# Kernel optimization log

Hardware: AMD Instinct MI355X
Metric: run time of the kernel (lower is better)

The kernel has to match this reference:

```python
import jax, jax.numpy as jnp
import numpy as np

B, S, D, H = 2, 2048, 1024, 16
HD = D // H  # head_dim = 64


def setup_inputs() -> dict:
    key = jax.random.key(0)
    ks = jax.random.split(key, 12)
    scale = 1.0 / np.sqrt(D)
    inp = {
        "query": jax.random.normal(ks[0], (B, S, D), jnp.float32),
        "key": jax.random.normal(ks[1], (B, S, D), jnp.float32),
        "value": jax.random.normal(ks[2], (B, S, D), jnp.float32),
        # causal mask, broadcast over batch and heads; masked_fill where mask == 0
        "mask": jnp.tril(jnp.ones((1, 1, S, S), dtype=bool)),
        "Wq": jax.random.normal(ks[3], (D, D), jnp.float32) * scale,
        "bq": jax.random.normal(ks[4], (D,), jnp.float32) * scale,
        "Wk": jax.random.normal(ks[5], (D, D), jnp.float32) * scale,
        "bk": jax.random.normal(ks[6], (D,), jnp.float32) * scale,
        "Wv": jax.random.normal(ks[7], (D, D), jnp.float32) * scale,
        "bv": jax.random.normal(ks[8], (D,), jnp.float32) * scale,
        "Wo": jax.random.normal(ks[9], (D, D), jnp.float32) * scale,
        "bo": jax.random.normal(ks[10], (D,), jnp.float32) * scale,
    }
    return inp


def reference(query, key, value, mask, Wq, bq, Wk, bk, Wv, bv, Wo, bo):
    b = query.shape[0]
    # QKV projections -> [B, H, S, HD]
    q = (query @ Wq + bq).reshape(b, -1, H, HD).transpose(0, 2, 1, 3)
    k = (key @ Wk + bk).reshape(b, -1, H, HD).transpose(0, 2, 1, 3)
    v = (value @ Wv + bv).reshape(b, -1, H, HD).transpose(0, 2, 1, 3)
    # scores: [B, H, Sq, Sk]
    scores = jnp.einsum("bhqd,bhkd->bhqk", q, k) / jnp.sqrt(jnp.float32(HD))
    scores = jnp.where(mask, scores, jnp.float32(-1e9))
    attn = jax.nn.softmax(scores, axis=-1)
    # dropout is identity in eval mode
    ctx = jnp.einsum("bhqk,bhkd->bhqd", attn, v)  # [B, H, Sq, HD]
    concat = ctx.transpose(0, 2, 1, 3).reshape(b, -1, D)
    return concat @ Wo + bo
```

## Files before the change

### kernel.cpp

```cpp
#include <hip/hip_runtime.h>

#define B_ 2
#define S_ 2048
#define D_ 1024
#define H_ 16
#define HD_ 64
#define Msz (B_*S_)

typedef __attribute__((ext_vector_type(8))) short  short8v;
typedef __attribute__((ext_vector_type(4))) float  float4v;
typedef __attribute__((ext_vector_type(4))) unsigned int uint4v;

__device__ static __forceinline__ unsigned short f2bf(float x) {
    union { float f; unsigned u; } v; v.f = x;
    unsigned r = v.u + 0x7fffu + ((v.u >> 16) & 1u);
    return (unsigned short)(r >> 16);
}
__device__ static __forceinline__ float bf2f(unsigned short b) {
    union { float f; unsigned u; } v; v.u = ((unsigned)b) << 16;
    return v.f;
}
__device__ static __forceinline__ void split2(float x, unsigned short& hi, unsigned short& lo) {
    hi = f2bf(x);
    lo = f2bf(x - bf2f(hi));
}

__device__ static __forceinline__ void gl_lds16(const void* g, void* l) {
    __builtin_amdgcn_global_load_lds(
        (const __attribute__((address_space(1))) void*)g,
        (__attribute__((address_space(3))) void*)l, 16, 0, 0);
}

__global__ __launch_bounds__(256) void conv_split(
    const float* __restrict__ in, unsigned short* __restrict__ hi,
    unsigned short* __restrict__ lo, int n4)
{
    const int i = blockIdx.x * 256 + threadIdx.x;
    if (i >= n4) return;
    const float4 x = ((const float4*)in)[i];
    ushort4 h, l;
    split2(x.x, h.x, l.x);
    split2(x.y, h.y, l.y);
    split2(x.z, h.z, l.z);
    split2(x.w, h.w, l.w);
    ((ushort4*)hi)[i] = h;
    ((ushort4*)lo)[i] = l;
}

__global__ __launch_bounds__(256) void conv_split_T(
    const float* __restrict__ W, unsigned short* __restrict__ thi,
    unsigned short* __restrict__ tlo, int R, int C)
{
    __shared__ float t[32][33];
    const int tid = threadIdx.x;
    const int r8 = tid >> 5, c = tid & 31;
    const int kbase = blockIdx.y * 32;
    const int nbase = blockIdx.x * 32;
#pragma unroll
    for (int i = 0; i < 4; ++i)
        t[r8 + i*8][c] = W[(size_t)(kbase + r8 + i*8) * C + nbase + c];
    __syncthreads();
#pragma unroll
    for (int i = 0; i < 4; ++i) {
        const int rr = r8 + i*8;
        const float v = t[c][rr];
        unsigned short h, l; split2(v, h, l);
        thi[(size_t)(nbase + rr) * R + kbase + c] = h;
        tlo[(size_t)(nbase + rr) * R + kbase + c] = l;
    }
}

__global__ __launch_bounds__(256) void gemm_mfma_split(
    const unsigned short* __restrict__ Ahi, const unsigned short* __restrict__ Alo,
    const unsigned short* __restrict__ Bthi, const unsigned short* __restrict__ Btlo,
    const float* __restrict__ bias, float* __restrict__ out,
    unsigned short* __restrict__ ohi, unsigned short* __restrict__ olo,
    int M, int N, int K, int mode, float scale)
{
    __shared__ unsigned short Ah[128][40], Al[128][40], Bh[64][40], Bl[64][40];

    const int tid  = threadIdx.x;
    const int lane = tid & 63;
    const int wave = tid >> 6;
    const int wr = wave >> 1, wc = wave & 1;
    const int m0 = blockIdx.x * 128, n0 = blockIdx.y * 64;

    float4v acc[4][2];
#pragma unroll
    for (int mi = 0; mi < 4; ++mi)
#pragma unroll
        for (int ni = 0; ni < 2; ++ni)
#pragma unroll
            for (int r = 0; r < 4; ++r) acc[mi][ni][r] = 0.f;

    const int mrow = lane & 15;
    const int kb8  = (lane >> 4) * 8;

    for (int k0 = 0; k0 < K; k0 += 32) {
        __syncthreads();
#pragma unroll
        for (int c2 = 0; c2 < 2; ++c2) {
            const int id  = tid + c2*256;
            const int row = id >> 2, ko = (id & 3) * 8;
            *(short8v*)&Ah[row][ko] = *(const short8v*)&Ahi[(size_t)(m0+row)*K + k0 + ko];
            *(short8v*)&Al[row][ko] = *(const short8v*)&Alo[(size_t)(m0+row)*K + k0 + ko];
        }
        {
            const int row = tid >> 2, ko = (tid & 3) * 8;
            *(short8v*)&Bh[row][ko] = *(const short8v*)&Bthi[(size_t)(n0+row)*K + k0 + ko];
            *(short8v*)&Bl[row][ko] = *(const short8v*)&Btlo[(size_t)(n0+row)*K + k0 + ko];
        }
        __syncthreads();

        short8v af[4][2], bfr[2][2];
#pragma unroll
        for (int mi = 0; mi < 4; ++mi) {
            af[mi][0] = *(const short8v*)&Ah[wr*64 + mi*16 + mrow][kb8];
            af[mi][1] = *(const short8v*)&Al[wr*64 + mi*16 + mrow][kb8];
        }
#pragma unroll
        for (int ni = 0; ni < 2; ++ni) {
            bfr[ni][0] = *(const short8v*)&Bh[wc*32 + ni*16 + mrow][kb8];
            bfr[ni][1] = *(const short8v*)&Bl[wc*32 + ni*16 + mrow][kb8];
        }
#pragma unroll
        for (int mi = 0; mi < 4; ++mi)
#pragma unroll
            for (int ni = 0; ni < 2; ++ni) {
                acc[mi][ni] = __builtin_amdgcn_mfma_f32_16x16x32_bf16(af[mi][0], bfr[ni][0], acc[mi][ni], 0, 0, 0);
                acc[mi][ni] = __builtin_amdgcn_mfma_f32_16x16x32_bf16(af[mi][0], bfr[ni][1], acc[mi][ni], 0, 0, 0);
                acc[mi][ni] = __builtin_amdgcn_mfma_f32_16x16x32_bf16(af[mi][1], bfr[ni][0], acc[mi][ni], 0, 0, 0);
            }
    }

    const int rbase = (lane >> 4) * 4, cidx = lane & 15;
#pragma unroll
    for (int mi = 0; mi < 4; ++mi)
#pragma unroll
        for (int ni = 0; ni < 2; ++ni) {
            const int col = n0 + wc*32 + ni*16 + cidx;
            const float bv = bias[col];
#pragma unroll
            for (int r = 0; r < 4; ++r) {
                const int row = m0 + wr*64 + mi*16 + rbase + r;
                const float v = (acc[mi][ni][r] + bv) * scale;
                if (mode == 0) {
                    out[(size_t)row * N + col] = v;
                } else {
                    const int bb = row >> 11;
                    const int ss = row & (S_ - 1);
                    const int hh = col >> 6;
                    const int hd = col & (HD_ - 1);
                    const size_t o = (((size_t)(bb*H_ + hh) * S_) + ss) * HD_ + hd;
                    unsigned short hb, lb; split2(v, hb, lb);
                    ohi[o] = hb;
                    olo[o] = lb;
                }
            }
        }
}

__global__ __launch_bounds__(256) void transpose_v(
    const unsigned short* __restrict__ V, unsigned short* __restrict__ Vt)
{
    __shared__ unsigned tbuf[64][33];
    const int tid = threadIdx.x;
    const int head = blockIdx.y;
    const int s0 = blockIdx.x * 64;
    const unsigned short* src = V + (size_t)head * S_ * HD_;
    unsigned short* dst = Vt + (size_t)head * HD_ * S_;

    const int sp = tid >> 3;
    const int dch = tid & 7;
    const short8v a = *(const short8v*)&src[(size_t)(s0 + 2*sp    ) * HD_ + dch*8];
    const short8v b = *(const short8v*)&src[(size_t)(s0 + 2*sp + 1) * HD_ + dch*8];
#pragma unroll
    for (int j = 0; j < 8; ++j) {
        const unsigned lo = (unsigned short)a[j];
        const unsigned hi = (unsigned short)b[j];
        tbuf[dch*8 + j][sp] = lo | (hi << 16);
    }
    __syncthreads();
#pragma unroll
    for (int i = 0; i < 2; ++i) {
        const int c = i*256 + tid;
        const int d = c >> 3, ch = c & 7;
        uint4v o;
#pragma unroll
        for (int k = 0; k < 4; ++k) o[k] = tbuf[d][ch*4 + k];
        *(uint4v*)&dst[(size_t)d * S_ + s0 + ch*8] = o;
    }
}

__global__ __launch_bounds__(256) void attn_mfma(
    const unsigned short* __restrict__ Qhi, const unsigned short* __restrict__ Qlo,
    const unsigned short* __restrict__ Khi, const unsigned short* __restrict__ Klo,
    const unsigned short* __restrict__ Vt,
    unsigned short* __restrict__ Chi, unsigned short* __restrict__ Clo)
{
    __shared__ unsigned short Ks[2][2][64][64];
    __shared__ unsigned short Vs[2][64][64];
    __shared__ unsigned short Ps[4][32][64];

    const int tid = threadIdx.x, lane = tid & 63, w = tid >> 6;
    const int bid = blockIdx.x;
    const int head = bid & 31;
    const int qb = ((bid >> 5) + head) & 15;
    const int q0 = qb * 128;

    const size_t hQK = (size_t)head * S_ * HD_;
    const unsigned short* Qh = Qhi + hQK;
    const unsigned short* Ql = Qlo + hQK;
    const unsigned short* Kh = Khi + hQK;
    const unsigned short* Kl = Klo + hQK;
    const unsigned short* Vth = Vt + (size_t)head * HD_ * S_;

    const int fr = lane & 15;
    const int fk = (lane >> 4) * 8;
    const int xorE = (lane & 7) * 8;
    const int rbase = (lane >> 4) * 4;

    short8v qf[2][2][2];
#pragma unroll
    for (int mi = 0; mi < 2; ++mi)
#pragma unroll
        for (int ks = 0; ks < 2; ++ks) {
            const size_t off = (size_t)(q0 + w*32 + mi*16 + fr) * HD_ + ks*32 + fk;
            qf[mi][ks][0] = *(const short8v*)&Qh[off];
            qf[mi][ks][1] = *(const short8v*)&Ql[off];
        }

    float4v oacc[2][4];
#pragma unroll
    for (int mi = 0; mi < 2; ++mi)
#pragma unroll
        for (int dt = 0; dt < 4; ++dt)
#pragma unroll
            for (int r = 0; r < 4; ++r) oacc[mi][dt][r] = 0.f;
    float m_run[2][4], l_run[2][4];
#pragma unroll
    for (int mi = 0; mi < 2; ++mi)
#pragma unroll
        for (int r = 0; r < 4; ++r) { m_run[mi][r] = -3.0e38f; l_run[mi][r] = 0.f; }

    const int srow = lane >> 3;
    const int sxor = ((lane & 7) ^ srow) * 8;

    const int ntiles = 2*qb + 2;
    const int last_t = 2*qb + (w >> 1);

    auto stage = [&](int t, int buf) {
#pragma unroll
        for (int cc = 0; cc < 6; ++cc) {
            const int c = w*6 + cc;
            if (c < 8) {
                gl_lds16(&Kh[(size_t)(t*64 + c*8 + srow)*HD_ + sxor], &Ks[buf][0][c*8][0]);
            } else if (c < 16) {
                const int c2 = c - 8;
                gl_lds16(&Kl[(size_t)(t*64 + c2*8 + srow)*HD_ + sxor], &Ks[buf][1][c2*8][0]);
            } else {
                const int c2 = c - 16;
                gl_lds16(&Vth[(size_t)(c2*8 + srow)*S_ + t*64 + sxor], &Vs[buf][c2*8][0]);
            }
        }
    };

    stage(0, 0);
    int buf = 0;
    for (int t = 0; t < ntiles; ++t) {
        if (t + 1 < ntiles) {
            stage(t + 1, buf ^ 1);
            asm volatile("s_waitcnt vmcnt(6)" ::: "memory");
        } else {
            asm volatile("s_waitcnt vmcnt(0)" ::: "memory");
        }
        __builtin_amdgcn_s_barrier();
        __builtin_amdgcn_sched_barrier(0);

        if (t <= last_t) {
            float4v sacc[2][4];
#pragma unroll
            for (int mi = 0; mi < 2; ++mi)
#pragma unroll
                for (int ni = 0; ni < 4; ++ni)
#pragma unroll
                    for (int r = 0; r < 4; ++r) sacc[mi][ni][r] = 0.f;
#pragma unroll
            for (int ks = 0; ks < 2; ++ks)
#pragma unroll
                for (int ni = 0; ni < 4; ++ni) {
                    const short8v kh = *(const short8v*)&Ks[buf][0][ni*16 + fr][(ks*32 + fk) ^ xorE];
                    const short8v kl = *(const short8v*)&Ks[buf][1][ni*16 + fr][(ks*32 + fk) ^ xorE];
#pragma unroll
                    for (int mi = 0; mi < 2; ++mi) {
                        sacc[mi][ni] = __builtin_amdgcn_mfma_f32_16x16x32_bf16(qf[mi][ks][0], kh, sacc[mi][ni], 0, 0, 0);
                        sacc[mi][ni] = __builtin_amdgcn_mfma_f32_16x16x32_bf16(qf[mi][ks][1], kh, sacc[mi][ni], 0, 0, 0);
                        sacc[mi][ni] = __builtin_amdgcn_mfma_f32_16x16x32_bf16(qf[mi][ks][0], kl, sacc[mi][ni], 0, 0, 0);
                    }
                }

            const int kvb = t*64;
            if (kvb + 63 > q0 + w*32) {
#pragma unroll
                for (int mi = 0; mi < 2; ++mi)
#pragma unroll
                    for (int ni = 0; ni < 4; ++ni)
#pragma unroll
                        for (int r = 0; r < 4; ++r) {
                            const int row_g = q0 + w*32 + mi*16 + rbase + r;
                            const int col_g = kvb + ni*16 + fr;
                            if (col_g > row_g) sacc[mi][ni][r] = -1.0e9f;
                        }
            }

            float tmax[2][4];
#pragma unroll
            for (int mi = 0; mi < 2; ++mi)
#pragma unroll
                for (int r = 0; r < 4; ++r)
                    tmax[mi][r] = fmaxf(fmaxf(sacc[mi][0][r], sacc[mi][1][r]),
                                        fmaxf(sacc[mi][2][r], sacc[mi][3][r]));
#pragma unroll
            for (int d = 1; d <= 8; d <<= 1)
#pragma unroll
                for (int mi = 0; mi < 2; ++mi)
#pragma unroll
                    for (int r = 0; r < 4; ++r)
                        tmax[mi][r] = fmaxf(tmax[mi][r], __shfl_xor(tmax[mi][r], d, 64));
#pragma unroll
            for (int mi = 0; mi < 2; ++mi)
#pragma unroll
                for (int r = 0; r < 4; ++r) {
                    const float mnew = fmaxf(m_run[mi][r], tmax[mi][r]);
                    const float sc = __expf(m_run[mi][r] - mnew);
                    m_run[mi][r] = mnew;
                    l_run[mi][r] *= sc;
#pragma unroll
                    for (int dt = 0; dt < 4; ++dt) oacc[mi][dt][r] *= sc;
                }
#pragma unroll
            for (int mi = 0; mi < 2; ++mi)
#pragma unroll
                for (int ni = 0; ni < 4; ++ni)
#pragma unroll
                    for (int r = 0; r < 4; ++r) {
                        const float p = __expf(sacc[mi][ni][r] - m_run[mi][r]);
                        const unsigned short pb = f2bf(p);
                        l_run[mi][r] += bf2f(pb);
                        const int R = mi*16 + rbase + r;
                        Ps[w][R][(ni*16 + fr) ^ ((R & 7) * 8)] = pb;
                    }

#pragma unroll
            for (int ks = 0; ks < 2; ++ks) {
                short8v pa[2];
#pragma unroll
                for (int mi = 0; mi < 2; ++mi)
                    pa[mi] = *(const short8v*)&Ps[w][mi*16 + fr][(ks*32 + fk) ^ xorE];
#pragma unroll
                for (int dt = 0; dt < 4; ++dt) {
                    const short8v vf = *(const short8v*)&Vs[buf][dt*16 + fr][(ks*32 + fk) ^ xorE];
#pragma unroll
                    for (int mi = 0; mi < 2; ++mi)
                        oacc[mi][dt] = __builtin_amdgcn_mfma_f32_16x16x32_bf16(pa[mi], vf, oacc[mi][dt], 0, 0, 0);
                }
            }
        }

        __builtin_amdgcn_s_barrier();
        buf ^= 1;
    }

#pragma unroll
    for (int d = 1; d <= 8; d <<= 1)
#pragma unroll
        for (int mi = 0; mi < 2; ++mi)
#pragma unroll
            for (int r = 0; r < 4; ++r)
                l_run[mi][r] += __shfl_xor(l_run[mi][r], d, 64);

    const int b = head >> 4, h = head & 15;
#pragma unroll
    for (int mi = 0; mi < 2; ++mi)
#pragma unroll
        for (int r = 0; r < 4; ++r) {
            const float inv = 1.0f / l_run[mi][r];
            const int sg = q0 + w*32 + mi*16 + rbase + r;
            const size_t rb = ((size_t)(b * S_ + sg)) * D_ + h * 64;
#pragma unroll
            for (int dt = 0; dt < 4; ++dt) {
                const float v = oacc[mi][dt][r] * inv;
                unsigned short hb, lb; split2(v, hb, lb);
                Chi[rb + dt*16 + fr] = hb;
                Clo[rb + dt*16 + fr] = lb;
            }
        }
}

extern "C" void kernel_launch(void* const* d_in, const int* in_sizes, int n_in,
                              void* d_out, int out_size, void* d_ws, size_t ws_size,
                              hipStream_t stream)
{
    const float* query = (const float*)d_in[0];
    const float* key   = (const float*)d_in[1];
    const float* value = (const float*)d_in[2];
    const float* Wq = (const float*)d_in[4];
    const float* bq = (const float*)d_in[5];
    const float* Wk = (const float*)d_in[6];
    const float* bk = (const float*)d_in[7];
    const float* Wv = (const float*)d_in[8];
    const float* bv = (const float*)d_in[9];
    const float* Wo = (const float*)d_in[10];
    const float* bo = (const float*)d_in[11];
    float* out = (float*)d_out;

    const size_t nElem = (size_t)B_ * S_ * D_;
    char* wsb = (char*)d_ws;
    unsigned short* Xhi = (unsigned short*)(wsb + 0);
    unsigned short* Xlo = (unsigned short*)(wsb + 8ull*1024*1024);
    unsigned short* Qph = (unsigned short*)(wsb + 16ull*1024*1024);
    unsigned short* Qpl = (unsigned short*)(wsb + 24ull*1024*1024);
    unsigned short* Kph = (unsigned short*)(wsb + 32ull*1024*1024);
    unsigned short* Kpl = (unsigned short*)(wsb + 40ull*1024*1024);
    unsigned short* Vph = (unsigned short*)(wsb + 48ull*1024*1024);
    unsigned short* Vpl = (unsigned short*)(wsb + 56ull*1024*1024);
    unsigned short* Wph = (unsigned short*)(wsb + 64ull*1024*1024);
    unsigned short* Wpl = (unsigned short*)(wsb + 66ull*1024*1024);
    unsigned short* VtT = Xhi;
    unsigned short* Chi = Vph;
    unsigned short* Clo = Vpl;

    const dim3 cblk(256);
    const dim3 cgrd(nElem / 1024);
    const dim3 tgrd(D_/32, D_/32);
    const dim3 ggrd(Msz/128, D_/64);
    const dim3 vtgrd(S_/64, B_*H_);
    const dim3 agrd(B_ * H_ * (S_/128));

    const float iscale = 0.125f;

    conv_split<<<cgrd, cblk, 0, stream>>>(query, Xhi, Xlo, (int)(nElem/4));
    conv_split_T<<<tgrd, cblk, 0, stream>>>(Wq, Wph, Wpl, D_, D_);
    gemm_mfma_split<<<ggrd, cblk, 0, stream>>>(Xhi, Xlo, Wph, Wpl, bq, nullptr, Qph, Qpl, Msz, D_, D_, 1, iscale);
    conv_split<<<cgrd, cblk, 0, stream>>>(key, Xhi, Xlo, (int)(nElem/4));
    conv_split_T<<<tgrd, cblk, 0, stream>>>(Wk, Wph, Wpl, D_, D_);
    gemm_mfma_split<<<ggrd, cblk, 0, stream>>>(Xhi, Xlo, Wph, Wpl, bk, nullptr, Kph, Kpl, Msz, D_, D_, 1, 1.0f);
    conv_split<<<cgrd, cblk, 0, stream>>>(value, Xhi, Xlo, (int)(nElem/4));
    conv_split_T<<<tgrd, cblk, 0, stream>>>(Wv, Wph, Wpl, D_, D_);
    gemm_mfma_split<<<ggrd, cblk, 0, stream>>>(Xhi, Xlo, Wph, Wpl, bv, nullptr, Vph, Vpl, Msz, D_, D_, 1, 1.0f);
    transpose_v<<<vtgrd, cblk, 0, stream>>>(Vph, VtT);
    attn_mfma<<<agrd, cblk, 0, stream>>>(Qph, Qpl, Kph, Kpl, VtT, Chi, Clo);
    conv_split_T<<<tgrd, cblk, 0, stream>>>(Wo, Wph, Wpl, D_, D_);
    gemm_mfma_split<<<ggrd, cblk, 0, stream>>>(Chi, Clo, Wph, Wpl, bo, out, nullptr, nullptr, Msz, D_, D_, 0, 1.0f);
}
```

Before: 421.8 us.

## Fuse fp32-to-bf16 split into GEMM A loads and widen GEMM tile to 128x128

Removes the separate conv_split kernels for query, key and value. The QKV GEMMs now read fp32 activations directly and split them into truncated-hi plus rounded-lo bf16 pairs while filling LDS. The GEMM tile also grows from 128x64 to 128x128, with each wave covering a 64x64 sub-tile, to raise reuse per LDS load. Together this drops three kernel launches and the intermediate hi/lo write and read-back. In exchange it uses more registers and LDS per block and launches half as many blocks, and the truncated hi split changes rounding slightly.

```diff
diff --git a/kernel.cpp b/kernel.cpp
--- a/kernel.cpp
+++ b/kernel.cpp
@@ -24,27 +24,16 @@
     hi = f2bf(x);
     lo = f2bf(x - bf2f(hi));
 }
+__device__ static __forceinline__ void split2t(float x, unsigned short& hi, unsigned short& lo) {
+    union { float f; unsigned u; } v; v.f = x;
+    hi = (unsigned short)(v.u >> 16);
+    lo = f2bf(x - bf2f(hi));
+}
 
 __device__ static __forceinline__ void gl_lds16(const void* g, void* l) {
     __builtin_amdgcn_global_load_lds(
         (const __attribute__((address_space(1))) void*)g,
         (__attribute__((address_space(3))) void*)l, 16, 0, 0);
-}
-
-__global__ __launch_bounds__(256) void conv_split(
-    const float* __restrict__ in, unsigned short* __restrict__ hi,
-    unsigned short* __restrict__ lo, int n4)
-{
-    const int i = blockIdx.x * 256 + threadIdx.x;
-    if (i >= n4) return;
-    const float4 x = ((const float4*)in)[i];
-    ushort4 h, l;
-    split2(x.x, h.x, l.x);
-    split2(x.y, h.y, l.y);
-    split2(x.z, h.z, l.z);
-    split2(x.w, h.w, l.w);
-    ((ushort4*)hi)[i] = h;
-    ((ushort4*)lo)[i] = l;
 }
 
 __global__ __launch_bounds__(256) void conv_split_T(
@@ -70,66 +59,90 @@
     }
 }
 
-__global__ __launch_bounds__(256) void gemm_mfma_split(
-    const unsigned short* __restrict__ Ahi, const unsigned short* __restrict__ Alo,
+template<int AMODE>
+__global__ __launch_bounds__(256) void gemm_mfma2(
+    const float* __restrict__ Af,
+    const unsigned short* __restrict__ Aphi, const unsigned short* __restrict__ Aplo,
     const unsigned short* __restrict__ Bthi, const unsigned short* __restrict__ Btlo,
     const float* __restrict__ bias, float* __restrict__ out,
     unsigned short* __restrict__ ohi, unsigned short* __restrict__ olo,
     int M, int N, int K, int mode, float scale)
 {
-    __shared__ unsigned short Ah[128][40], Al[128][40], Bh[64][40], Bl[64][40];
+    __shared__ __align__(16) unsigned short Ah[128][40], Al[128][40];
+    __shared__ __align__(16) unsigned short Bh[128][40], Bl[128][40];
 
     const int tid  = threadIdx.x;
     const int lane = tid & 63;
     const int wave = tid >> 6;
     const int wr = wave >> 1, wc = wave & 1;
-    const int m0 = blockIdx.x * 128, n0 = blockIdx.y * 64;
-
-    float4v acc[4][2];
+    const int m0 = blockIdx.x * 128, n0 = blockIdx.y * 128;
+
+    float4v acc[4][4];
 #pragma unroll
     for (int mi = 0; mi < 4; ++mi)
 #pragma unroll
-        for (int ni = 0; ni < 2; ++ni)
+        for (int ni = 0; ni < 4; ++ni)
 #pragma unroll
             for (int r = 0; r < 4; ++r) acc[mi][ni][r] = 0.f;
 
-    const int mrow = lane & 15;
-    const int kb8  = (lane >> 4) * 8;
+    const int fr  = lane & 15;
+    const int kb8 = (lane >> 4) * 8;
 
     for (int k0 = 0; k0 < K; k0 += 32) {
         __syncthreads();
-#pragma unroll
-        for (int c2 = 0; c2 < 2; ++c2) {
-            const int id  = tid + c2*256;
-            const int row = id >> 2, ko = (id & 3) * 8;
-            *(short8v*)&Ah[row][ko] = *(const short8v*)&Ahi[(size_t)(m0+row)*K + k0 + ko];
-            *(short8v*)&Al[row][ko] = *(const short8v*)&Alo[(size_t)(m0+row)*K + k0 + ko];
-        }
-        {
-            const int row = tid >> 2, ko = (tid & 3) * 8;
-            *(short8v*)&Bh[row][ko] = *(const short8v*)&Bthi[(size_t)(n0+row)*K + k0 + ko];
-            *(short8v*)&Bl[row][ko] = *(const short8v*)&Btlo[(size_t)(n0+row)*K + k0 + ko];
+        if (AMODE == 0) {
+#pragma unroll
+            for (int it = 0; it < 4; ++it) {
+                const int id  = tid + it*256;
+                const int row = id >> 3;
+                const int kq  = (id & 7) * 4;
+                const float4 f = *(const float4*)&Af[(size_t)(m0+row)*K + k0 + kq];
+                ushort4 h, l;
+                split2t(f.x, h.x, l.x);
+                split2t(f.y, h.y, l.y);
+                split2t(f.z, h.z, l.z);
+                split2t(f.w, h.w, l.w);
+                *(ushort4*)&Ah[row][kq] = h;
+                *(ushort4*)&Al[row][kq] = l;
+            }
+        } else {
+#pragma unroll
+            for (int it = 0; it < 2; ++it) {
+                const int id  = tid + it*256;
+                const int row = id >> 2;
+                const int kc  = (id & 3) * 8;
+                *(short8v*)&Ah[row][kc] = *(const short8v*)&Aphi[(size_t)(m0+row)*K + k0 + kc];
+                *(short8v*)&Al[row][kc] = *(const short8v*)&Aplo[(size_t)(m0+row)*K + k0 + kc];
+            }
+        }
+#pragma unroll
+        for (int it = 0; it < 2; ++it) {
+            const int id  = tid + it*256;
+            const int row = id >> 2;
+            const int kc  = (id & 3) * 8;
+            *(short8v*)&Bh[row][kc] = *(const short8v*)&Bthi[(size_t)(n0+row)*K + k0 + kc];
+            *(short8v*)&Bl[row][kc] = *(const short8v*)&Btlo[(size_t)(n0+row)*K + k0 + kc];
         }
         __syncthreads();
 
-        short8v af[4][2], bfr[2][2];
+        short8v af[4][2], bf[4][2];
 #pragma unroll
         for (int mi = 0; mi < 4; ++mi) {
-            af[mi][0] = *(const short8v*)&Ah[wr*64 + mi*16 + mrow][kb8];
-            af[mi][1] = *(const short8v*)&Al[wr*64 + mi*16 + mrow][kb8];
-        }
-#pragma unroll
-        for (int ni = 0; ni < 2; ++ni) {
-            bfr[ni][0] = *(const short8v*)&Bh[wc*32 + ni*16 + mrow][kb8];
-            bfr[ni][1] = *(const short8v*)&Bl[wc*32 + ni*16 + mrow][kb8];
+            af[mi][0] = *(const short8v*)&Ah[wr*64 + mi*16 + fr][kb8];
+            af[mi][1] = *(const short8v*)&Al[wr*64 + mi*16 + fr][kb8];
+        }
+#pragma unroll
+        for (int ni = 0; ni < 4; ++ni) {
+            bf[ni][0] = *(const short8v*)&Bh[wc*64 + ni*16 + fr][kb8];
+            bf[ni][1] = *(const short8v*)&Bl[wc*64 + ni*16 + fr][kb8];
         }
 #pragma unroll
         for (int mi = 0; mi < 4; ++mi)
 #pragma unroll
-            for (int ni = 0; ni < 2; ++ni) {
-                acc[mi][ni] = __builtin_amdgcn_mfma_f32_16x16x32_bf16(af[mi][0], bfr[ni][0], acc[mi][ni], 0, 0, 0);
-                acc[mi][ni] = __builtin_amdgcn_mfma_f32_16x16x32_bf16(af[mi][0], bfr[ni][1], acc[mi][ni], 0, 0, 0);
-                acc[mi][ni] = __builtin_amdgcn_mfma_f32_16x16x32_bf16(af[mi][1], bfr[ni][0], acc[mi][ni], 0, 0, 0);
+            for (int ni = 0; ni < 4; ++ni) {
+                acc[mi][ni] = __builtin_amdgcn_mfma_f32_16x16x32_bf16(af[mi][0], bf[ni][0], acc[mi][ni], 0, 0, 0);
+                acc[mi][ni] = __builtin_amdgcn_mfma_f32_16x16x32_bf16(af[mi][0], bf[ni][1], acc[mi][ni], 0, 0, 0);
+                acc[mi][ni] = __builtin_amdgcn_mfma_f32_16x16x32_bf16(af[mi][1], bf[ni][0], acc[mi][ni], 0, 0, 0);
             }
     }
 
@@ -137,8 +150,8 @@
 #pragma unroll
     for (int mi = 0; mi < 4; ++mi)
 #pragma unroll
-        for (int ni = 0; ni < 2; ++ni) {
-            const int col = n0 + wc*32 + ni*16 + cidx;
+        for (int ni = 0; ni < 4; ++ni) {
+            const int col = n0 + wc*64 + ni*16 + cidx;
             const float bv = bias[col];
 #pragma unroll
             for (int r = 0; r < 4; ++r) {
@@ -414,42 +427,39 @@
     const float* bo = (const float*)d_in[11];
     float* out = (float*)d_out;
 
-    const size_t nElem = (size_t)B_ * S_ * D_;
     char* wsb = (char*)d_ws;
-    unsigned short* Xhi = (unsigned short*)(wsb + 0);
-    unsigned short* Xlo = (unsigned short*)(wsb + 8ull*1024*1024);
-    unsigned short* Qph = (unsigned short*)(wsb + 16ull*1024*1024);
-    unsigned short* Qpl = (unsigned short*)(wsb + 24ull*1024*1024);
-    unsigned short* Kph = (unsigned short*)(wsb + 32ull*1024*1024);
-    unsigned short* Kpl = (unsigned short*)(wsb + 40ull*1024*1024);
-    unsigned short* Vph = (unsigned short*)(wsb + 48ull*1024*1024);
-    unsigned short* Vpl = (unsigned short*)(wsb + 56ull*1024*1024);
-    unsigned short* Wph = (unsigned short*)(wsb + 64ull*1024*1024);
-    unsigned short* Wpl = (unsigned short*)(wsb + 66ull*1024*1024);
-    unsigned short* VtT = Xhi;
+    unsigned short* Qph = (unsigned short*)(wsb + 0);
+    unsigned short* Qpl = (unsigned short*)(wsb + 8ull*1024*1024);
+    unsigned short* Kph = (unsigned short*)(wsb + 16ull*1024*1024);
+    unsigned short* Kpl = (unsigned short*)(wsb + 24ull*1024*1024);
+    unsigned short* Vph = (unsigned short*)(wsb + 32ull*1024*1024);
+    unsigned short* Vpl = (unsigned short*)(wsb + 40ull*1024*1024);
+    unsigned short* VtT = (unsigned short*)(wsb + 48ull*1024*1024);
+    unsigned short* Wph = (unsigned short*)(wsb + 56ull*1024*1024);
+    unsigned short* Wpl = (unsigned short*)(wsb + 58ull*1024*1024);
     unsigned short* Chi = Vph;
     unsigned short* Clo = Vpl;
 
     const dim3 cblk(256);
-    const dim3 cgrd(nElem / 1024);
     const dim3 tgrd(D_/32, D_/32);
-    const dim3 ggrd(Msz/128, D_/64);
+    const dim3 ggrd(Msz/128, D_/128);
     const dim3 vtgrd(S_/64, B_*H_);
     const dim3 agrd(B_ * H_ * (S_/128));
 
     const float iscale = 0.125f;
 
-    conv_split<<<cgrd, cblk, 0, stream>>>(query, Xhi, Xlo, (int)(nElem/4));
     conv_split_T<<<tgrd, cblk, 0, stream>>>(Wq, Wph, Wpl, D_, D_);
-    gemm_mfma_split<<<ggrd, cblk, 0, stream>>>(Xhi, Xlo, Wph, Wpl, bq, nullptr, Qph, Qpl, Msz, D_, D_, 1, iscale);
-    conv_split<<<cgrd, cblk, 0, stream>>>(key, Xhi, Xlo, (int)(nElem/4));
+    gemm_mfma2<0><<<ggrd, cblk, 0, stream>>>(query, nullptr, nullptr, Wph, Wpl, bq,
+                                             nullptr, Qph, Qpl, Msz, D_, D_, 1, iscale);
     conv_split_T<<<tgrd, cblk, 0, stream>>>(Wk, Wph, Wpl, D_, D_);
-    gemm_mfma_split<<<ggrd, cblk, 0, stream>>>(Xhi, Xlo, Wph, Wpl, bk, nullptr, Kph, Kpl, Msz, D_, D_, 1, 1.0f);
-    conv_split<<<cgrd, cblk, 0, stream>>>(value, Xhi, Xlo, (int)(nElem/4));
+    gemm_mfma2<0><<<ggrd, cblk, 0, stream>>>(key, nullptr, nullptr, Wph, Wpl, bk,
+                                             nullptr, Kph, Kpl, Msz, D_, D_, 1, 1.0f);
     conv_split_T<<<tgrd, cblk, 0, stream>>>(Wv, Wph, Wpl, D_, D_);
-    gemm_mfma_split<<<ggrd, cblk, 0, stream>>>(Xhi, Xlo, Wph, Wpl, bv, nullptr, Vph, Vpl, Msz, D_, D_, 1, 1.0f);
+    gemm_mfma2<0><<<ggrd, cblk, 0, stream>>>(value, nullptr, nullptr, Wph, Wpl, bv,
+                                             nullptr, Vph, Vpl, Msz, D_, D_, 1, 1.0f);
     transpose_v<<<vtgrd, cblk, 0, stream>>>(Vph, VtT);
     attn_mfma<<<agrd, cblk, 0, stream>>>(Qph, Qpl, Kph, Kpl, VtT, Chi, Clo);
     conv_split_T<<<tgrd, cblk, 0, stream>>>(Wo, Wph, Wpl, D_, D_);
-    gemm_mfma_split<<<ggrd, cblk, 0, stream>>>(Chi, Clo, Wph, Wpl, bo, out, nullptr, nullptr, Msz, D_, D_, 0, 1.0f);
-}
+    gemm_mfma2<1><<<ggrd, cblk, 0, stream>>>(nullptr, Chi, Clo, Wph, Wpl, bo,
+                                             out, nullptr, nullptr, Msz, D_, D_, 0, 1.0f);
+}
```

New measurement: 477.4 us. 1.13x slower.

## Rewrite split-bf16 GEMM with 128x128 tiles, direct global-to-LDS loads and XOR swizzle

Applied to the files above, without the earlier changes.

Replaces the projection GEMM with a 512-thread kernel that uses 128x128 output tiles and a K step of 64. Operands go from global memory straight into LDS through a gl_lds16 helper, and an XOR-swizzled layout is meant to avoid bank conflicts. The aim is fewer blocks, more reuse of each loaded tile, and fewer load instructions and barriers per K. The helper gl_lds16 is not defined in the shown diff, so the change depends on it already existing; there is still no double buffering.

```diff
diff --git a/kernel.cpp b/kernel.cpp
--- a/kernel.cpp
+++ b/kernel.cpp
@@ -70,20 +70,21 @@
     }
 }
 
-__global__ __launch_bounds__(256) void gemm_mfma_split(
-    const unsigned short* __restrict__ Ahi, const unsigned short* __restrict__ Alo,
+__global__ __launch_bounds__(512) void gemm3(
+    const unsigned short* __restrict__ Aphi, const unsigned short* __restrict__ Aplo,
     const unsigned short* __restrict__ Bthi, const unsigned short* __restrict__ Btlo,
     const float* __restrict__ bias, float* __restrict__ out,
     unsigned short* __restrict__ ohi, unsigned short* __restrict__ olo,
     int M, int N, int K, int mode, float scale)
 {
-    __shared__ unsigned short Ah[128][40], Al[128][40], Bh[64][40], Bl[64][40];
+    __shared__ __align__(16) unsigned short Ah[128][64], Al[128][64];
+    __shared__ __align__(16) unsigned short Bh[128][64], Bl[128][64];
 
     const int tid  = threadIdx.x;
     const int lane = tid & 63;
-    const int wave = tid >> 6;
-    const int wr = wave >> 1, wc = wave & 1;
-    const int m0 = blockIdx.x * 128, n0 = blockIdx.y * 64;
+    const int w    = tid >> 6;
+    const int wr = w >> 2, wc = w & 3;
+    const int m0 = blockIdx.x * 128, n0 = blockIdx.y * 128;
 
     float4v acc[4][2];
 #pragma unroll
@@ -93,44 +94,56 @@
 #pragma unroll
             for (int r = 0; r < 4; ++r) acc[mi][ni][r] = 0.f;
 
-    const int mrow = lane & 15;
-    const int kb8  = (lane >> 4) * 8;
-
-    for (int k0 = 0; k0 < K; k0 += 32) {
+    const int fr   = lane & 15;
+    const int fk   = (lane >> 4) * 8;
+    const int xorE = (lane & 7) * 8;
+    const int srow = lane >> 3;
+    const int sxor = ((lane & 7) ^ srow) * 8;
+
+    const int bufsel = w >> 1;
+    const int gbase  = (w & 1) * 8;
+
+    for (int k0 = 0; k0 < K; k0 += 64) {
+#pragma unroll
+        for (int i = 0; i < 8; ++i) {
+            const int row0 = (gbase + i) * 8;
+            const int grow = row0 + srow;
+            if (bufsel == 0)
+                gl_lds16(&Aphi[(size_t)(m0+grow)*K + k0 + sxor], &Ah[row0][0]);
+            else if (bufsel == 1)
+                gl_lds16(&Aplo[(size_t)(m0+grow)*K + k0 + sxor], &Al[row0][0]);
+            else if (bufsel == 2)
+                gl_lds16(&Bthi[(size_t)(n0+grow)*K + k0 + sxor], &Bh[row0][0]);
+            else
+                gl_lds16(&Btlo[(size_t)(n0+grow)*K + k0 + sxor], &Bl[row0][0]);
+        }
         __syncthreads();
-#pragma unroll
-        for (int c2 = 0; c2 < 2; ++c2) {
-            const int id  = tid + c2*256;
-            const int row = id >> 2, ko = (id & 3) * 8;
-            *(short8v*)&Ah[row][ko] = *(const short8v*)&Ahi[(size_t)(m0+row)*K + k0 + ko];
-            *(short8v*)&Al[row][ko] = *(const short8v*)&Alo[(size_t)(m0+row)*K + k0 + ko];
-        }
-        {
-            const int row = tid >> 2, ko = (tid & 3) * 8;
-            *(short8v*)&Bh[row][ko] = *(const short8v*)&Bthi[(size_t)(n0+row)*K + k0 + ko];
-            *(short8v*)&Bl[row][ko] = *(const short8v*)&Btlo[(size_t)(n0+row)*K + k0 + ko];
+
+#pragma unroll
+        for (int ks = 0; ks < 2; ++ks) {
+            short8v af[4][2], bf[2][2];
+#pragma unroll
+            for (int mi = 0; mi < 4; ++mi) {
+                const int row = wr*64 + mi*16 + fr;
+                af[mi][0] = *(const short8v*)&Ah[row][(ks*32 + fk) ^ xorE];
+                af[mi][1] = *(const short8v*)&Al[row][(ks*32 + fk) ^ xorE];
+            }
+#pragma unroll
+            for (int ni = 0; ni < 2; ++ni) {
+                const int row = wc*32 + ni*16 + fr;
+                bf[ni][0] = *(const short8v*)&Bh[row][(ks*32 + fk) ^ xorE];
+                bf[ni][1] = *(const short8v*)&Bl[row][(ks*32 + fk) ^ xorE];
+            }
+#pragma unroll
+            for (int mi = 0; mi < 4; ++mi)
+#pragma unroll
+                for (int ni = 0; ni < 2; ++ni) {
+                    acc[mi][ni] = __builtin_amdgcn_mfma_f32_16x16x32_bf16(af[mi][0], bf[ni][0], acc[mi][ni], 0, 0, 0);
+                    acc[mi][ni] = __builtin_amdgcn_mfma_f32_16x16x32_bf16(af[mi][0], bf[ni][1], acc[mi][ni], 0, 0, 0);
+                    acc[mi][ni] = __builtin_amdgcn_mfma_f32_16x16x32_bf16(af[mi][1], bf[ni][0], acc[mi][ni], 0, 0, 0);
+                }
         }
         __syncthreads();
-
-        short8v af[4][2], bfr[2][2];
-#pragma unroll
-        for (int mi = 0; mi < 4; ++mi) {
-            af[mi][0] = *(const short8v*)&Ah[wr*64 + mi*16 + mrow][kb8];
-            af[mi][1] = *(const short8v*)&Al[wr*64 + mi*16 + mrow][kb8];
-        }
-#pragma unroll
-        for (int ni = 0; ni < 2; ++ni) {
-            bfr[ni][0] = *(const short8v*)&Bh[wc*32 + ni*16 + mrow][kb8];
-            bfr[ni][1] = *(const short8v*)&Bl[wc*32 + ni*16 + mrow][kb8];
-        }
-#pragma unroll
-        for (int mi = 0; mi < 4; ++mi)
-#pragma unroll
-            for (int ni = 0; ni < 2; ++ni) {
-                acc[mi][ni] = __builtin_amdgcn_mfma_f32_16x16x32_bf16(af[mi][0], bfr[ni][0], acc[mi][ni], 0, 0, 0);
-                acc[mi][ni] = __builtin_amdgcn_mfma_f32_16x16x32_bf16(af[mi][0], bfr[ni][1], acc[mi][ni], 0, 0, 0);
-                acc[mi][ni] = __builtin_amdgcn_mfma_f32_16x16x32_bf16(af[mi][1], bfr[ni][0], acc[mi][ni], 0, 0, 0);
-            }
     }
 
     const int rbase = (lane >> 4) * 4, cidx = lane & 15;
@@ -431,9 +444,10 @@
     unsigned short* Clo = Vpl;
 
     const dim3 cblk(256);
+    const dim3 gblk(512);
     const dim3 cgrd(nElem / 1024);
     const dim3 tgrd(D_/32, D_/32);
-    const dim3 ggrd(Msz/128, D_/64);
+    const dim3 ggrd(Msz/128, D_/128);
     const dim3 vtgrd(S_/64, B_*H_);
     const dim3 agrd(B_ * H_ * (S_/128));
 
@@ -441,15 +455,15 @@
 
     conv_split<<<cgrd, cblk, 0, stream>>>(query, Xhi, Xlo, (int)(nElem/4));
     conv_split_T<<<tgrd, cblk, 0, stream>>>(Wq, Wph, Wpl, D_, D_);
-    gemm_mfma_split<<<ggrd, cblk, 0, stream>>>(Xhi, Xlo, Wph, Wpl, bq, nullptr, Qph, Qpl, Msz, D_, D_, 1, iscale);
+    gemm3<<<ggrd, gblk, 0, stream>>>(Xhi, Xlo, Wph, Wpl, bq, nullptr, Qph, Qpl, Msz, D_, D_, 1, iscale);
     conv_split<<<cgrd, cblk, 0, stream>>>(key, Xhi, Xlo, (int)(nElem/4));
     conv_split_T<<<tgrd, cblk, 0, stream>>>(Wk, Wph, Wpl, D_, D_);
-    gemm_mfma_split<<<ggrd, cblk, 0, stream>>>(Xhi, Xlo, Wph, Wpl, bk, nullptr, Kph, Kpl, Msz, D_, D_, 1, 1.0f);
+    gemm3<<<ggrd, gblk, 0, stream>>>(Xhi, Xlo, Wph, Wpl, bk, nullptr, Kph, Kpl, Msz, D_, D_, 1, 1.0f);
     conv_split<<<cgrd, cblk, 0, stream>>>(value, Xhi, Xlo, (int)(nElem/4));
     conv_split_T<<<tgrd, cblk, 0, stream>>>(Wv, Wph, Wpl, D_, D_);
-    gemm_mfma_split<<<ggrd, cblk, 0, stream>>>(Xhi, Xlo, Wph, Wpl, bv, nullptr, Vph, Vpl, Msz, D_, D_, 1, 1.0f);
+    gemm3<<<ggrd, gblk, 0, stream>>>(Xhi, Xlo, Wph, Wpl, bv, nullptr, Vph, Vpl, Msz, D_, D_, 1, 1.0f);
     transpose_v<<<vtgrd, cblk, 0, stream>>>(Vph, VtT);
     attn_mfma<<<agrd, cblk, 0, stream>>>(Qph, Qpl, Kph, Kpl, VtT, Chi, Clo);
     conv_split_T<<<tgrd, cblk, 0, stream>>>(Wo, Wph, Wpl, D_, D_);
-    gemm_mfma_split<<<ggrd, cblk, 0, stream>>>(Chi, Clo, Wph, Wpl, bo, out, nullptr, nullptr, Msz, D_, D_, 0, 1.0f);
-}
+    gemm3<<<ggrd, gblk, 0, stream>>>(Chi, Clo, Wph, Wpl, bo, out, nullptr, nullptr, Msz, D_, D_, 0, 1.0f);
+}
```

Measured after the change: 447.9 us. 6.2% more time.
